# Kernel optimization log

Measured on AMD Instinct MI355X. Metric: run time of the kernel, lower is better.

The kernel has to match this reference:

```python
import jax, jax.numpy as jnp
import numpy as np

N = 2048      # oscillators
K = 8         # neighbors per oscillator (connectivity0)
B = 32        # batch
T = 20        # time_steps
EPS0 = 1.0    # update_rate
ANNEAL = 0.0  # anneal


def setup_inputs() -> dict:
    key = jax.random.key(0)
    k1, k2, k3 = jax.random.split(key, 3)
    coupling = jax.random.normal(k1, (B, N, K), dtype=jnp.float32)
    connectivity = jax.random.randint(k2, (N, K), 0, N)
    phase0 = 2.0 * jnp.pi * jax.random.uniform(k3, (B, N), dtype=jnp.float32)
    omega = jnp.zeros((B, N), dtype=jnp.float32)
    return {"coupling": coupling, "phase0": phase0, "omega": omega,
            "connectivity": connectivity}


def reference(coupling, phase0, omega, connectivity):
    # Scatter sparse per-neighbor couplings [B,N,K] into dense [B,N,N]
    # (torch scatter_ dim=2 with the same index per batch element).
    rows = jnp.arange(N)[:, None]                      # [N,1]
    C = jnp.zeros((B, N, N), coupling.dtype).at[:, rows, connectivity].set(coupling)
    # n = number of nonzero couplings per row  [B,N]
    n = jnp.abs(jnp.sign(C)).sum(axis=2)

    def step(carry, i):
        phase, eps = carry                             # phase [B,N]
        s, c = jnp.sin(phase), jnp.cos(phase)
        Cs = jnp.einsum('bnm,bm->bn', C, s)
        Cc = jnp.einsum('bnm,bm->bn', C, c)
        delta = eps * (Cs * c - Cc * s) / n
        phase_new = phase + delta + omega
        # eps_anneal called after each update with step index i
        eps_new = eps - ANNEAL * i.astype(eps.dtype) * eps / T
        return (phase_new, eps_new), phase_new

    (_, _), phases = jax.lax.scan(step, (phase0, jnp.float32(EPS0)), jnp.arange(T))
    # phase_list: initial phase followed by T updated phases  [T+1,B,N]
    return jnp.concatenate([phase0[None], phases], axis=0)
```

## Files before the change

kernel.cpp:

```cpp
#include <hip/hip_runtime.h>

#define NN 2048
#define KK 8
#define BB 32
#define TT 20

__global__ __launch_bounds__(1024) void osci_kernel(
    const float* __restrict__ coupling,
    const float* __restrict__ phase0,
    const float* __restrict__ omega,
    const int*   __restrict__ conn,
    float*       __restrict__ out)
{
    const int b   = blockIdx.x;
    const int tid = threadIdx.x;

    __shared__ float ph_buf[2][NN];

    int   cidx[2][KK];
    float w[2][KK];
    float inv_n[2];
    float om[2];
    float ph[2];

    for (int t = 0; t < 2; ++t) {
        const int i = tid + t * 1024;
        float p = phase0[b * NN + i];
        ph[t] = p;
        ph_buf[0][i] = p;
        out[(size_t)b * NN + i] = p;
        om[t] = omega[b * NN + i];

        int   jj[KK];
        float vv[KK];
        #pragma unroll
        for (int k = 0; k < KK; ++k) {
            jj[k] = conn[i * KK + k];
            vv[k] = coupling[((size_t)b * NN + i) * KK + k];
        }
        int cnt = 0;
        #pragma unroll
        for (int k = 0; k < KK; ++k) {
            bool over = false;
            #pragma unroll
            for (int k2 = k + 1; k2 < KK; ++k2) over = over || (jj[k2] == jj[k]);
            if (over) vv[k] = 0.0f;
            if (vv[k] != 0.0f) ++cnt;
        }
        #pragma unroll
        for (int k = 0; k < KK; ++k) { cidx[t][k] = jj[k]; w[t][k] = vv[k]; }
        inv_n[t] = 1.0f / (float)cnt;
    }
    __syncthreads();

    for (int step = 0; step < TT; ++step) {
        const int cur = step & 1;
        const int nxt = cur ^ 1;
        #pragma unroll
        for (int t = 0; t < 2; ++t) {
            const int i = tid + t * 1024;
            float acc = 0.0f;
            #pragma unroll
            for (int k = 0; k < KK; ++k) {
                const float pj = ph_buf[cur][cidx[t][k]];
                acc += w[t][k] * __sinf(pj - ph[t]);
            }
            const float pn = ph[t] + acc * inv_n[t] + om[t];
            ph[t] = pn;
            ph_buf[nxt][i] = pn;
            out[((size_t)(step + 1) * BB + b) * NN + i] = pn;
        }
        __syncthreads();
    }
}

extern "C" void kernel_launch(void* const* d_in, const int* in_sizes, int n_in,
                              void* d_out, int out_size, void* d_ws, size_t ws_size,
                              hipStream_t stream) {
    const float* coupling = (const float*)d_in[0];
    const float* phase0   = (const float*)d_in[1];
    const float* omega    = (const float*)d_in[2];
    const int*   conn     = (const int*)d_in[3];
    float* out = (float*)d_out;

    osci_kernel<<<BB, 1024, 0, stream>>>(coupling, phase0, omega, conn, out);
}
```

Before: 80.99 us.

## Split each batch across four workgroups with global-memory flag barriers per step

Each batch element is now handled by four 512-thread workgroups, each owning a quarter of the oscillators, which raises the grid from 32 to 128 blocks so more compute units are used. After every time step the groups exchange phases through the output buffer and synchronise with an atomic counter spin-barrier in workspace memory, which is cleared by a memset before launch. This adds a cross-workgroup global barrier and global reloads on every step. It also relies on all 128 blocks being resident at the same time to avoid deadlock.

```diff
diff --git a/kernel.cpp b/kernel.cpp
--- a/kernel.cpp
+++ b/kernel.cpp
@@ -4,33 +4,38 @@
 #define KK 8
 #define BB 32
 #define TT 20
+#define GG 4
+#define CHUNK (NN / GG)
 
-__global__ __launch_bounds__(1024) void osci_kernel(
+__global__ __launch_bounds__(CHUNK) void osci_kernel(
     const float* __restrict__ coupling,
     const float* __restrict__ phase0,
     const float* __restrict__ omega,
     const int*   __restrict__ conn,
-    float*       __restrict__ out)
+    float*       __restrict__ out,
+    unsigned*    __restrict__ flags)
 {
-    const int b   = blockIdx.x;
+    const int b   = blockIdx.x & (BB - 1);
+    const int c   = blockIdx.x >> 5;
     const int tid = threadIdx.x;
+    const int i   = c * CHUNK + tid;
 
-    __shared__ float ph_buf[2][NN];
+    __shared__ float ph_buf[NN];
 
-    int   cidx[2][KK];
-    float w[2][KK];
-    float inv_n[2];
-    float om[2];
-    float ph[2];
+    #pragma unroll
+    for (int r = 0; r < GG; ++r) {
+        const int idx = tid + r * CHUNK;
+        ph_buf[idx] = phase0[b * NN + idx];
+    }
 
-    for (int t = 0; t < 2; ++t) {
-        const int i = tid + t * 1024;
-        float p = phase0[b * NN + i];
-        ph[t] = p;
-        ph_buf[0][i] = p;
-        out[(size_t)b * NN + i] = p;
-        om[t] = omega[b * NN + i];
+    float ph = phase0[b * NN + i];
+    out[(size_t)b * NN + i] = ph;
+    const float om = omega[b * NN + i];
 
+    int   cidx[KK];
+    float w[KK];
+    float inv_n;
+    {
         int   jj[KK];
         float vv[KK];
         #pragma unroll
@@ -48,28 +53,43 @@
             if (vv[k] != 0.0f) ++cnt;
         }
         #pragma unroll
-        for (int k = 0; k < KK; ++k) { cidx[t][k] = jj[k]; w[t][k] = vv[k]; }
-        inv_n[t] = 1.0f / (float)cnt;
+        for (int k = 0; k < KK; ++k) { cidx[k] = jj[k]; w[k] = vv[k]; }
+        inv_n = 1.0f / (float)cnt;
     }
     __syncthreads();
 
-    for (int step = 0; step < TT; ++step) {
-        const int cur = step & 1;
-        const int nxt = cur ^ 1;
+    #pragma unroll 1
+    for (int t = 0; t < TT; ++t) {
+        float* outrow = out + ((size_t)(t + 1) * BB + b) * NN;
+
+        float acc = 0.0f;
         #pragma unroll
-        for (int t = 0; t < 2; ++t) {
-            const int i = tid + t * 1024;
-            float acc = 0.0f;
-            #pragma unroll
-            for (int k = 0; k < KK; ++k) {
-                const float pj = ph_buf[cur][cidx[t][k]];
-                acc += w[t][k] * __sinf(pj - ph[t]);
-            }
-            const float pn = ph[t] + acc * inv_n[t] + om[t];
-            ph[t] = pn;
-            ph_buf[nxt][i] = pn;
-            out[((size_t)(step + 1) * BB + b) * NN + i] = pn;
+        for (int k = 0; k < KK; ++k) {
+            const float pj = ph_buf[cidx[k]];
+            acc += w[k] * __sinf(pj - ph);
         }
+        const float pn = ph + acc * inv_n + om;
+        ph = pn;
+        __hip_atomic_store(&outrow[i], pn, __ATOMIC_RELAXED, __HIP_MEMORY_SCOPE_AGENT);
+
+        if (t == TT - 1) break;
+
+        __syncthreads();
+        if (tid == 0) {
+            unsigned* f = &flags[b * TT + t];
+            __hip_atomic_fetch_add(f, 1u, __ATOMIC_ACQ_REL, __HIP_MEMORY_SCOPE_AGENT);
+            while (__hip_atomic_load(f, __ATOMIC_ACQUIRE, __HIP_MEMORY_SCOPE_AGENT) < GG) {}
+        }
+        __syncthreads();
+
+        #pragma unroll
+        for (int r = 0; r < GG; ++r) {
+            if (r == c) continue;
+            const int idx = tid + r * CHUNK;
+            ph_buf[idx] = __hip_atomic_load(&outrow[idx], __ATOMIC_RELAXED,
+                                            __HIP_MEMORY_SCOPE_AGENT);
+        }
+        ph_buf[i] = pn;
         __syncthreads();
     }
 }
@@ -83,5 +103,7 @@
     const int*   conn     = (const int*)d_in[3];
     float* out = (float*)d_out;
 
-    osci_kernel<<<BB, 1024, 0, stream>>>(coupling, phase0, omega, conn, out);
+    hipMemsetAsync(d_ws, 0, BB * TT * sizeof(unsigned), stream);
+    osci_kernel<<<BB * GG, CHUNK, 0, stream>>>(coupling, phase0, omega, conn, out,
+                                               (unsigned*)d_ws);
 }
```

Result: slower. 132.6 us (+63.7%).
